# Kernel tuning notes

Hardware: AMD Instinct MI355X
Metric: run time of the kernel (lower is better)

The kernel has to match this reference:

```python
import jax, jax.numpy as jnp
import numpy as np

EPS = 1e-5
INV_SQRT2 = 0.7071067811865476

def _rmsnorm(x, w):
    rms = jnp.sqrt(jnp.sum(x * x, axis=-1) / x.shape[-1] + EPS)
    return x / rms[..., None] * w

def _gelu(x):
    # exact erf-based GELU as in the torch module
    return x * (1.0 + jax.scipy.special.erf(x * INV_SQRT2)) * 0.5

def setup_inputs() -> dict:
    key = jax.random.key(0)
    ks = jax.random.split(key, 8)
    B, S, D, DFF = 4, 2048, 1024, 4096
    s = 0.02  # realistic init scale keeps softmax non-degenerate
    return {
        "x": jax.random.normal(ks[0], (B, S, D), jnp.float32),
        "ln1": jax.random.uniform(ks[1], (D,), jnp.float32),
        "ln2": jax.random.uniform(ks[2], (D,), jnp.float32),
        "ffn1": jax.random.normal(ks[3], (DFF, D), jnp.float32) * s,
        "ffn2": jax.random.normal(ks[4], (D, DFF), jnp.float32) * s,
        "k_proj": jax.random.normal(ks[5], (D, D), jnp.float32) * s,
        "q_proj": jax.random.normal(ks[6], (D, D), jnp.float32) * s,
        "v_proj": jax.random.normal(ks[7], (D, D), jnp.float32) * s,
        "out_proj": jax.random.normal(jax.random.fold_in(key, 99), (D, D), jnp.float32) * s,
    }

def reference(x, ln1, ln2, ffn1, ffn2, k_proj, q_proj, v_proj, out_proj):
    S = x.shape[1]
    d_k = x.shape[-1]
    # --- attention branch (single-head, as in source) ---
    h = _rmsnorm(x, ln1)
    Q = h @ q_proj.T  # [B,S,D]
    K = h @ k_proj.T
    V = h @ v_proj.T
    scores = jnp.einsum('bqd,bkd->bqk', Q, K) / jnp.sqrt(jnp.float32(d_k))
    attn = jax.nn.softmax(scores, axis=-1)
    # source: softmax first, then zero out strict-upper (future) entries, renormalize
    causal = jnp.tril(jnp.ones((S, S), jnp.float32))
    attn = attn * causal
    attn = attn / jnp.sum(attn, axis=-1, keepdims=True)
    mh = jnp.einsum('bqk,bkd->bqd', attn, V) @ out_proj
    y = x + mh
    # --- FFN branch: NOTE source feeds RMSNorm2(x), not y ---
    h2 = _rmsnorm(x, ln2)
    ff = _gelu(h2 @ ffn1.T) @ ffn2.T
    return y + ff
```

## Files before the change

kernel.cpp:

```cpp
#include <hip/hip_runtime.h>
#include <math.h>

typedef __bf16 bf16_t;
typedef __bf16 bf16x8 __attribute__((ext_vector_type(8)));
typedef float f32x4 __attribute__((ext_vector_type(4)));

#define LDS16(g, l) __builtin_amdgcn_global_load_lds( \
    (__attribute__((address_space(1))) void*)(g),     \
    (__attribute__((address_space(3))) void*)(l), 16, 0, 0)

__global__ __launch_bounds__(256) void prep_kernel(
    const float* __restrict__ qp, const float* __restrict__ kp,
    const float* __restrict__ vp, const float* __restrict__ f1,
    const float* __restrict__ f2, const float* __restrict__ op,
    const float* __restrict__ x, const float* __restrict__ ln1,
    bf16_t* __restrict__ qkvb, bf16_t* __restrict__ f1b,
    bf16_t* __restrict__ f2b, bf16_t* __restrict__ opT,
    bf16_t* __restrict__ h1)
{
    __shared__ float tile[32][33];
    __shared__ float red[4];
    int bid = blockIdx.x;
    int t = threadIdx.x;
    if (bid < 11264) {
        size_t i = ((size_t)bid * 256 + t) * 4;
        const float* src;
        bf16_t* dst;
        if (i < 3145728) {
            if (i < 1048576)      { src = qp + i;             dst = qkvb + i; }
            else if (i < 2097152) { src = kp + (i - 1048576); dst = qkvb + i; }
            else                  { src = vp + (i - 2097152); dst = qkvb + i; }
        } else if (i < 7340032) { src = f1 + (i - 3145728); dst = f1b + (i - 3145728); }
        else                    { src = f2 + (i - 7340032); dst = f2b + (i - 7340032); }
        float4 v = *(const float4*)src;
        dst[0] = (bf16_t)v.x; dst[1] = (bf16_t)v.y;
        dst[2] = (bf16_t)v.z; dst[3] = (bf16_t)v.w;
    } else if (bid < 12288) {
        int b2 = bid - 11264;
        int c0 = (b2 & 31) * 32, r0 = (b2 >> 5) * 32;
        int tx = t & 31, ty = t >> 5;
#pragma unroll
        for (int i = 0; i < 32; i += 8)
            tile[ty + i][tx] = op[(size_t)(r0 + ty + i) * 1024 + c0 + tx];
        __syncthreads();
#pragma unroll
        for (int i = 0; i < 32; i += 8)
            opT[(size_t)(c0 + ty + i) * 1024 + r0 + tx] = (bf16_t)tile[tx][ty + i];
    } else {
        int row = bid - 12288;
        float4 xv = ((const float4*)(x + (size_t)row * 1024))[t];
        float ss = xv.x * xv.x + xv.y * xv.y + xv.z * xv.z + xv.w * xv.w;
#pragma unroll
        for (int o = 32; o > 0; o >>= 1) ss += __shfl_xor(ss, o, 64);
        if ((t & 63) == 0) red[t >> 6] = ss;
        __syncthreads();
        ss = red[0] + red[1] + red[2] + red[3];
        float rinv = rsqrtf(ss * (1.0f / 1024.0f) + 1e-5f);
        float4 wv = ((const float4*)ln1)[t];
        bf16_t* hp = h1 + (size_t)row * 1024 + t * 4;
        hp[0] = (bf16_t)(xv.x * rinv * wv.x);
        hp[1] = (bf16_t)(xv.y * rinv * wv.y);
        hp[2] = (bf16_t)(xv.z * rinv * wv.z);
        hp[3] = (bf16_t)(xv.w * rinv * wv.w);
    }
}

__global__ __launch_bounds__(256) void rmsnorm_kernel(
    const float* __restrict__ x, const float* __restrict__ w,
    bf16_t* __restrict__ h)
{
    int row = blockIdx.x;
    int t = threadIdx.x;
    float4 xv = ((const float4*)(x + (size_t)row * 1024))[t];
    float ss = xv.x * xv.x + xv.y * xv.y + xv.z * xv.z + xv.w * xv.w;
#pragma unroll
    for (int o = 32; o > 0; o >>= 1) ss += __shfl_xor(ss, o, 64);
    __shared__ float red[4];
    if ((t & 63) == 0) red[t >> 6] = ss;
    __syncthreads();
    ss = red[0] + red[1] + red[2] + red[3];
    float rinv = rsqrtf(ss * (1.0f / 1024.0f) + 1e-5f);
    float4 wv = ((const float4*)w)[t];
    bf16_t* hp = h + (size_t)row * 1024 + t * 4;
    hp[0] = (bf16_t)(xv.x * rinv * wv.x);
    hp[1] = (bf16_t)(xv.y * rinv * wv.y);
    hp[2] = (bf16_t)(xv.z * rinv * wv.z);
    hp[3] = (bf16_t)(xv.w * rinv * wv.w);
}

__global__ __launch_bounds__(256) void transpose_bf16(
    const bf16_t* __restrict__ in, bf16_t* __restrict__ out,
    int rows, int ldin, long long sIn, long long sOut)
{
    __shared__ bf16_t tile[32][33];
    int b = blockIdx.z;
    const bf16_t* ip = in + (long long)b * sIn;
    bf16_t* op = out + (long long)b * sOut;
    int c0 = blockIdx.x * 32, r0 = blockIdx.y * 32;
    int tx = threadIdx.x & 31, ty = threadIdx.x >> 5;
#pragma unroll
    for (int i = 0; i < 32; i += 8)
        tile[ty + i][tx] = ip[(size_t)(r0 + ty + i) * ldin + c0 + tx];
    __syncthreads();
#pragma unroll
    for (int i = 0; i < 32; i += 8)
        op[(size_t)(c0 + ty + i) * rows + r0 + tx] = tile[tx][ty + i];
}

__global__ __launch_bounds__(256) void causal_softmax_kernel(bf16_t* __restrict__ SP)
{
    const int S = 2048;
    int q = blockIdx.x, b = blockIdx.y;
    bf16_t* row = SP + ((size_t)b * S + q) * S;
    int t = threadIdx.x;
    int j0 = t * 8;
    int Jstore = ((q >> 7) + 1) << 7;

    float v[8];
    if (j0 + 7 <= q) {
        bf16x8 xv = *(const bf16x8*)(row + j0);
#pragma unroll
        for (int i = 0; i < 8; i++) v[i] = (float)xv[i];
    } else if (j0 <= q) {
#pragma unroll
        for (int i = 0; i < 8; i++)
            v[i] = (j0 + i <= q) ? (float)row[j0 + i] : -1e30f;
    } else {
#pragma unroll
        for (int i = 0; i < 8; i++) v[i] = -1e30f;
    }

    float mx = v[0];
#pragma unroll
    for (int i = 1; i < 8; i++) mx = fmaxf(mx, v[i]);
#pragma unroll
    for (int o = 32; o > 0; o >>= 1) mx = fmaxf(mx, __shfl_xor(mx, o, 64));
    __shared__ float sm[4], ssum[4];
    if ((t & 63) == 0) sm[t >> 6] = mx;
    __syncthreads();
    mx = fmaxf(fmaxf(sm[0], sm[1]), fmaxf(sm[2], sm[3]));

    float e[8];
    float sum = 0.f;
#pragma unroll
    for (int i = 0; i < 8; i++) {
        e[i] = (v[i] > -1e29f) ? expf(v[i] - mx) : 0.f;
        sum += e[i];
    }
#pragma unroll
    for (int o = 32; o > 0; o >>= 1) sum += __shfl_xor(sum, o, 64);
    if ((t & 63) == 0) ssum[t >> 6] = sum;
    __syncthreads();
    sum = ssum[0] + ssum[1] + ssum[2] + ssum[3];
    float r = 1.0f / sum;

    if (j0 < Jstore) {
        bf16x8 ov;
#pragma unroll
        for (int i = 0; i < 8; i++) ov[i] = (bf16_t)(e[i] * r);
        *(bf16x8*)(row + j0) = ov;
    }
}

template <int EPI, bool CSKIP, bool CKLOOP, bool ASPLIT>
__global__ __launch_bounds__(256) void gemm_bt(
    const bf16_t* __restrict__ A, const bf16_t* __restrict__ A2, int lda,
    const bf16_t* __restrict__ B, int ldb,
    void* Cv, int ldc, const float* R,
    int K, int Ksp, int Mt, long long sA, long long sB, long long sC,
    float scale)
{
    int id = blockIdx.x, bz = blockIdx.z;
    int xcd = id & 7, p = id >> 3;
    int chunk = Mt >> 3;
    int bm = xcd * chunk + (p % chunk);
    int bn = p / chunk;
    if (CSKIP && bn > bm) return;

    __shared__ __align__(16) bf16_t At[128 * 64];
    __shared__ __align__(16) bf16_t Bt[128 * 64];
    int t = threadIdx.x;
    int w = t >> 6, l = t & 63;
    int wm = w >> 1, wn = w & 1;
    int lane_m = l & 15, quad = l >> 4;

    const bf16_t* Ag = A + (long long)bz * sA + (size_t)(bm * 128) * lda;
    const bf16_t* Bg = B + (long long)bz * sB + (size_t)(bn * 128) * ldb;

    int Keff = K;
    if (CKLOOP) {
        int kk = (bm + 1) * 128;
        if (kk < K) Keff = kk;
    }

    f32x4 acc[4][4] = {};

    int rb = w * 8 + (l >> 3);
    int g0 = ((l & 7) ^ ((l >> 3) & 7)) * 8;
    const bf16_t* a0[4];
    const bf16_t* a1[4];
    const bf16_t* b0[4];
#pragma unroll
    for (int j = 0; j < 4; j++) {
        size_t ro = (size_t)(rb + 32 * j);
        a0[j] = Ag + ro * lda + g0;
        if (ASPLIT) a1[j] = A2 + (long long)bz * sA + (size_t)(bm * 128) * lda
                           + ro * lda + g0;
        b0[j] = Bg + ro * ldb + g0;
    }

    int s0 = (quad ^ (lane_m & 7)) * 8;
    int s1 = ((4 + quad) ^ (lane_m & 7)) * 8;

    for (int kt = 0; kt < Keff; kt += 64) {
        __syncthreads();
#pragma unroll
        for (int j = 0; j < 4; j++) {
            const bf16_t* pa = a0[j] + kt;
            if (ASPLIT && kt >= Ksp) pa = a1[j] + (kt - Ksp);
            LDS16(pa, At + (size_t)w * 512 + j * 2048);
            LDS16(b0[j] + kt, Bt + (size_t)w * 512 + j * 2048);
        }
        __syncthreads();

#pragma unroll
        for (int h = 0; h < 2; h++) {
            int sh = h ? s1 : s0;
            bf16x8 af[4], bfr[4];
#pragma unroll
            for (int mi = 0; mi < 4; mi++)
                af[mi] = *(const bf16x8*)(At + (wm * 64 + mi * 16 + lane_m) * 64 + sh);
#pragma unroll
            for (int ni = 0; ni < 4; ni++)
                bfr[ni] = *(const bf16x8*)(Bt + (wn * 64 + ni * 16 + lane_m) * 64 + sh);
#pragma unroll
            for (int mi = 0; mi < 4; mi++)
#pragma unroll
                for (int ni = 0; ni < 4; ni++)
                    acc[mi][ni] = __builtin_amdgcn_mfma_f32_16x16x32_bf16(
                        af[mi], bfr[ni], acc[mi][ni], 0, 0, 0);
        }
    }

    long long cbase = (long long)bz * sC;
#pragma unroll
    for (int mi = 0; mi < 4; mi++) {
#pragma unroll
        for (int r = 0; r < 4; r++) {
            int row = bm * 128 + wm * 64 + mi * 16 + quad * 4 + r;
#pragma unroll
            for (int ni = 0; ni < 4; ni++) {
                int col = bn * 128 + wn * 64 + ni * 16 + lane_m;
                float v = acc[mi][ni][r];
                size_t idx = (size_t)(cbase + (long long)row * ldc + col);
                if (EPI == 0) {
                    ((bf16_t*)Cv)[idx] = (bf16_t)(v * scale);
                } else if (EPI == 1) {
                    float g = 0.5f * v * (1.0f + erff(v * 0.70710678118654752f));
                    ((bf16_t*)Cv)[idx] = (bf16_t)g;
                } else {
                    float rv = R[(size_t)row * ldc + col];
                    ((float*)Cv)[idx] = v + rv;
                }
            }
        }
    }
}

extern "C" void kernel_launch(void* const* d_in, const int* in_sizes, int n_in,
                              void* d_out, int out_size, void* d_ws, size_t ws_size,
                              hipStream_t stream)
{
    (void)in_sizes; (void)n_in; (void)out_size;
    const float* x    = (const float*)d_in[0];
    const float* ln1  = (const float*)d_in[1];
    const float* ln2  = (const float*)d_in[2];
    const float* ffn1 = (const float*)d_in[3];
    const float* ffn2 = (const float*)d_in[4];
    const float* kp   = (const float*)d_in[5];
    const float* qp   = (const float*)d_in[6];
    const float* vp   = (const float*)d_in[7];
    const float* op   = (const float*)d_in[8];
    float* out = (float*)d_out;

    const size_t MiB = 1048576;
    char* ws = (char*)d_ws;
    bf16_t* qkvb = (bf16_t*)(ws + 0 * MiB);
    bf16_t* opT  = (bf16_t*)(ws + 6 * MiB);
    bf16_t* f1b  = (bf16_t*)(ws + 8 * MiB);
    bf16_t* f2b  = (bf16_t*)(ws + 16 * MiB);
    bf16_t* h1   = (bf16_t*)(ws + 24 * MiB);
    bf16_t* VT   = (bf16_t*)(ws + 24 * MiB);
    bf16_t* h2   = (bf16_t*)(ws + 24 * MiB);
    bf16_t* QKVb = (bf16_t*)(ws + 40 * MiB);
    bf16_t* AV   = (bf16_t*)(ws + 40 * MiB);
    bf16_t* G0   = (bf16_t*)(ws + 40 * MiB);
    bf16_t* G1   = (bf16_t*)(ws + 72 * MiB);
    bf16_t* SP   = (bf16_t*)d_out;
    bool bigws = ws_size >= 104 * MiB;

    dim3 blk(256);
    const int HUGE_K = 1 << 30;

    prep_kernel<<<dim3(20480), blk, 0, stream>>>(
        qp, kp, vp, ffn1, ffn2, op, x, ln1, qkvb, f1b, f2b, opT, h1);

    gemm_bt<0, false, false, false><<<dim3(1536), blk, 0, stream>>>(
        h1, h1, 1024, qkvb, 1024, QKVb, 3072, nullptr,
        1024, HUGE_K, 64, 0, 0, 0, 1.0f);

    gemm_bt<0, true, false, false><<<dim3(256, 1, 4), blk, 0, stream>>>(
        QKVb, QKVb, 3072, QKVb + 1024, 3072, SP, 2048, nullptr,
        1024, HUGE_K, 16,
        (long long)2048 * 3072, (long long)2048 * 3072, (long long)2048 * 2048,
        1.0f / 32.0f);

    transpose_bf16<<<dim3(32, 64, 4), blk, 0, stream>>>(
        QKVb + 2048, VT, 2048, 3072,
        (long long)2048 * 3072, (long long)1024 * 2048);

    causal_softmax_kernel<<<dim3(2048, 4), blk, 0, stream>>>(SP);

    gemm_bt<0, false, true, false><<<dim3(128, 1, 4), blk, 0, stream>>>(
        SP, SP, 2048, VT, 2048, AV, 1024, nullptr,
        2048, HUGE_K, 16,
        (long long)2048 * 2048, (long long)1024 * 2048, (long long)2048 * 1024,
        1.0f);

    gemm_bt<2, false, false, false><<<dim3(512), blk, 0, stream>>>(
        AV, AV, 1024, opT, 1024, out, 1024, x,
        1024, HUGE_K, 64, 0, 0, 0, 1.0f);

    rmsnorm_kernel<<<dim3(8192), blk, 0, stream>>>(x, ln2, h2);

    if (bigws) {
        gemm_bt<1, false, false, false><<<dim3(1024), blk, 0, stream>>>(
            h2, h2, 1024, f1b, 1024, G0, 2048, nullptr,
            1024, HUGE_K, 64, 0, 0, 0, 1.0f);
        gemm_bt<1, false, false, false><<<dim3(1024), blk, 0, stream>>>(
            h2, h2, 1024, f1b + (size_t)2048 * 1024, 1024, G1, 2048, nullptr,
            1024, HUGE_K, 64, 0, 0, 0, 1.0f);
        gemm_bt<2, false, false, true><<<dim3(512), blk, 0, stream>>>(
            G0, G1, 2048, f2b, 4096, out, 1024, out,
            4096, 2048, 64, 0, 0, 0, 1.0f);
    } else {
        for (int half = 0; half < 2; half++) {
            gemm_bt<1, false, false, false><<<dim3(1024), blk, 0, stream>>>(
                h2, h2, 1024, f1b + (size_t)half * 2048 * 1024, 1024, G0, 2048,
                nullptr, 1024, HUGE_K, 64, 0, 0, 0, 1.0f);
            gemm_bt<2, false, false, false><<<dim3(512), blk, 0, stream>>>(
                G0, G0, 2048, f2b + half * 2048, 4096, out, 1024, out,
                2048, HUGE_K, 64, 0, 0, 0, 1.0f);
        }
    }
}
```

Measured before the change: 546.7 us.

## Add 8-wave 256x128 GEMM kernel with XCD-aware mapping for dense projections

Adds a new 512-thread GEMM kernel using 256x128 tiles, double-buffered direct-to-LDS loads interleaved with four MFMA phases, priority raising and an XCD-aware block-to-tile mapping. It replaces the QKV, out-projection and FFN GEMMs in the big-workspace path, and merges the two FFN1 halves into a single launch writing a contiguous G buffer. Larger tiles raise operand reuse and the interleaved prefetch aims to hide global latency. The cost is more LDS and registers per block and reliance on hardcoded grid shapes matching M/N.

```diff
diff --git a/kernel.cpp b/kernel.cpp
--- a/kernel.cpp
+++ b/kernel.cpp
@@ -267,6 +267,165 @@
     }
 }
 
+template <int EPI>
+__global__ __launch_bounds__(512, 2) void gemm8p(
+    const bf16_t* __restrict__ A, int lda,
+    const bf16_t* __restrict__ B, int ldb,
+    void* Cv, int ldc, const float* R, int K, float scale)
+{
+    int id = blockIdx.x;
+    int xcd = id & 7, p = id >> 3;
+    int bm = xcd * 4 + (p & 3);
+    int bn = p >> 2;
+
+    __shared__ __align__(16) bf16_t As[2][256 * 64];
+    __shared__ __align__(16) bf16_t Bs[2][128 * 64];
+
+    int t = threadIdx.x;
+    int w = t >> 6, l = t & 63;
+    int wm = w >> 1, wn = w & 1;
+    int lane_m = l & 15, quad = l >> 4;
+
+    const bf16_t* Ag = A + (size_t)(bm * 256) * lda;
+    const bf16_t* Bg = B + (size_t)(bn * 128) * ldb;
+
+    int rsub = w * 8 + (l >> 3);
+    int g0 = ((l & 7) ^ ((l >> 3) & 7)) * 8;
+    const bf16_t* pA0 = Ag + (size_t)(rsub)       * lda + g0;
+    const bf16_t* pA1 = Ag + (size_t)(64 + rsub)  * lda + g0;
+    const bf16_t* pA2 = Ag + (size_t)(128 + rsub) * lda + g0;
+    const bf16_t* pA3 = Ag + (size_t)(192 + rsub) * lda + g0;
+    const bf16_t* pB0 = Bg + (size_t)(rsub)       * ldb + g0;
+    const bf16_t* pB1 = Bg + (size_t)(64 + rsub)  * ldb + g0;
+
+    int sl0 = (quad ^ (lane_m & 7)) * 8;
+    int sl1 = ((4 + quad) ^ (lane_m & 7)) * 8;
+    int arow = (wm * 64 + lane_m) * 64;
+    int brow = (wn * 64 + lane_m) * 64;
+
+    f32x4 acc[4][4] = {};
+
+    LDS16(pA0, &As[0][0 * 4096 + w * 512]);
+    LDS16(pA1, &As[0][1 * 4096 + w * 512]);
+    LDS16(pA2, &As[0][2 * 4096 + w * 512]);
+    LDS16(pA3, &As[0][3 * 4096 + w * 512]);
+    LDS16(pB0, &Bs[0][0 * 4096 + w * 512]);
+    LDS16(pB1, &Bs[0][1 * 4096 + w * 512]);
+    asm volatile("s_waitcnt vmcnt(0)" ::: "memory");
+    __builtin_amdgcn_s_barrier();
+
+    int cur = 0;
+    for (int kt = 0; kt < K; kt += 64) {
+        const bool pf = (kt + 64) < K;
+        const int nxt = cur ^ 1;
+        const bf16_t* Ac = As[cur];
+        const bf16_t* Bc = Bs[cur];
+        bf16x8 af[2], bfr0[4], bfr1[4];
+
+        af[0] = *(const bf16x8*)(Ac + arow + 0 * 1024 + sl0);
+        af[1] = *(const bf16x8*)(Ac + arow + 1 * 1024 + sl0);
+#pragma unroll
+        for (int ni = 0; ni < 4; ni++)
+            bfr0[ni] = *(const bf16x8*)(Bc + brow + ni * 1024 + sl0);
+        if (pf) {
+            LDS16(pA0 + kt + 64, &As[nxt][0 * 4096 + w * 512]);
+            LDS16(pA1 + kt + 64, &As[nxt][1 * 4096 + w * 512]);
+            LDS16(pA2 + kt + 64, &As[nxt][2 * 4096 + w * 512]);
+            LDS16(pA3 + kt + 64, &As[nxt][3 * 4096 + w * 512]);
+        }
+        __builtin_amdgcn_s_barrier();
+        asm volatile("s_waitcnt lgkmcnt(0)" ::: "memory");
+        __builtin_amdgcn_sched_barrier(0);
+        __builtin_amdgcn_s_setprio(1);
+#pragma unroll
+        for (int j = 0; j < 2; j++)
+#pragma unroll
+            for (int ni = 0; ni < 4; ni++)
+                acc[j][ni] = __builtin_amdgcn_mfma_f32_16x16x32_bf16(
+                    af[j], bfr0[ni], acc[j][ni], 0, 0, 0);
+        __builtin_amdgcn_s_setprio(0);
+        __builtin_amdgcn_s_barrier();
+
+        af[0] = *(const bf16x8*)(Ac + arow + 0 * 1024 + sl1);
+        af[1] = *(const bf16x8*)(Ac + arow + 1 * 1024 + sl1);
+#pragma unroll
+        for (int ni = 0; ni < 4; ni++)
+            bfr1[ni] = *(const bf16x8*)(Bc + brow + ni * 1024 + sl1);
+        if (pf) {
+            LDS16(pB0 + kt + 64, &Bs[nxt][0 * 4096 + w * 512]);
+            LDS16(pB1 + kt + 64, &Bs[nxt][1 * 4096 + w * 512]);
+        }
+        __builtin_amdgcn_s_barrier();
+        asm volatile("s_waitcnt lgkmcnt(0)" ::: "memory");
+        __builtin_amdgcn_sched_barrier(0);
+        __builtin_amdgcn_s_setprio(1);
+#pragma unroll
+        for (int j = 0; j < 2; j++)
+#pragma unroll
+            for (int ni = 0; ni < 4; ni++)
+                acc[j][ni] = __builtin_amdgcn_mfma_f32_16x16x32_bf16(
+                    af[j], bfr1[ni], acc[j][ni], 0, 0, 0);
+        __builtin_amdgcn_s_setprio(0);
+        __builtin_amdgcn_s_barrier();
+
+        af[0] = *(const bf16x8*)(Ac + arow + 2 * 1024 + sl0);
+        af[1] = *(const bf16x8*)(Ac + arow + 3 * 1024 + sl0);
+        __builtin_amdgcn_s_barrier();
+        asm volatile("s_waitcnt lgkmcnt(0)" ::: "memory");
+        __builtin_amdgcn_sched_barrier(0);
+        __builtin_amdgcn_s_setprio(1);
+#pragma unroll
+        for (int j = 0; j < 2; j++)
+#pragma unroll
+            for (int ni = 0; ni < 4; ni++)
+                acc[2 + j][ni] = __builtin_amdgcn_mfma_f32_16x16x32_bf16(
+                    af[j], bfr0[ni], acc[2 + j][ni], 0, 0, 0);
+        __builtin_amdgcn_s_setprio(0);
+        __builtin_amdgcn_s_barrier();
+
+        af[0] = *(const bf16x8*)(Ac + arow + 2 * 1024 + sl1);
+        af[1] = *(const bf16x8*)(Ac + arow + 3 * 1024 + sl1);
+        __builtin_amdgcn_s_barrier();
+        asm volatile("s_waitcnt lgkmcnt(0)" ::: "memory");
+        __builtin_amdgcn_sched_barrier(0);
+        __builtin_amdgcn_s_setprio(1);
+#pragma unroll
+        for (int j = 0; j < 2; j++)
+#pragma unroll
+            for (int ni = 0; ni < 4; ni++)
+                acc[2 + j][ni] = __builtin_amdgcn_mfma_f32_16x16x32_bf16(
+                    af[j], bfr1[ni], acc[2 + j][ni], 0, 0, 0);
+        __builtin_amdgcn_s_setprio(0);
+        if (pf) asm volatile("s_waitcnt vmcnt(0)" ::: "memory");
+        __builtin_amdgcn_s_barrier();
+
+        cur = nxt;
+    }
+
+#pragma unroll
+    for (int mi = 0; mi < 4; mi++) {
+#pragma unroll
+        for (int r = 0; r < 4; r++) {
+            int row = bm * 256 + wm * 64 + mi * 16 + quad * 4 + r;
+#pragma unroll
+            for (int ni = 0; ni < 4; ni++) {
+                int col = bn * 128 + wn * 64 + ni * 16 + lane_m;
+                float v = acc[mi][ni][r];
+                size_t idx = (size_t)row * ldc + col;
+                if (EPI == 0) {
+                    ((bf16_t*)Cv)[idx] = (bf16_t)(v * scale);
+                } else if (EPI == 1) {
+                    float g = 0.5f * v * (1.0f + erff(v * 0.70710678118654752f));
+                    ((bf16_t*)Cv)[idx] = (bf16_t)g;
+                } else {
+                    float rv = R[(size_t)row * ldc + col];
+                    ((float*)Cv)[idx] = v + rv;
+                }
+            }
+        }
+    }
+}
+
 extern "C" void kernel_launch(void* const* d_in, const int* in_sizes, int n_in,
                               void* d_out, int out_size, void* d_ws, size_t ws_size,
                               hipStream_t stream)
@@ -295,19 +454,18 @@
     bf16_t* QKVb = (bf16_t*)(ws + 40 * MiB);
     bf16_t* AV   = (bf16_t*)(ws + 40 * MiB);
     bf16_t* G0   = (bf16_t*)(ws + 40 * MiB);
-    bf16_t* G1   = (bf16_t*)(ws + 72 * MiB);
     bf16_t* SP   = (bf16_t*)d_out;
     bool bigws = ws_size >= 104 * MiB;
 
     dim3 blk(256);
+    dim3 blk8(512);
     const int HUGE_K = 1 << 30;
 
     prep_kernel<<<dim3(20480), blk, 0, stream>>>(
         qp, kp, vp, ffn1, ffn2, op, x, ln1, qkvb, f1b, f2b, opT, h1);
 
-    gemm_bt<0, false, false, false><<<dim3(1536), blk, 0, stream>>>(
-        h1, h1, 1024, qkvb, 1024, QKVb, 3072, nullptr,
-        1024, HUGE_K, 64, 0, 0, 0, 1.0f);
+    gemm8p<0><<<dim3(768), blk8, 0, stream>>>(
+        h1, 1024, qkvb, 1024, QKVb, 3072, nullptr, 1024, 1.0f);
 
     gemm_bt<0, true, false, false><<<dim3(256, 1, 4), blk, 0, stream>>>(
         QKVb, QKVb, 3072, QKVb + 1024, 3072, SP, 2048, nullptr,
@@ -327,22 +485,16 @@
         (long long)2048 * 2048, (long long)1024 * 2048, (long long)2048 * 1024,
         1.0f);
 
-    gemm_bt<2, false, false, false><<<dim3(512), blk, 0, stream>>>(
-        AV, AV, 1024, opT, 1024, out, 1024, x,
-        1024, HUGE_K, 64, 0, 0, 0, 1.0f);
+    gemm8p<2><<<dim3(256), blk8, 0, stream>>>(
+        AV, 1024, opT, 1024, out, 1024, x, 1024, 1.0f);
 
     rmsnorm_kernel<<<dim3(8192), blk, 0, stream>>>(x, ln2, h2);
 
     if (bigws) {
-        gemm_bt<1, false, false, false><<<dim3(1024), blk, 0, stream>>>(
-            h2, h2, 1024, f1b, 1024, G0, 2048, nullptr,
-            1024, HUGE_K, 64, 0, 0, 0, 1.0f);
-        gemm_bt<1, false, false, false><<<dim3(1024), blk, 0, stream>>>(
-            h2, h2, 1024, f1b + (size_t)2048 * 1024, 1024, G1, 2048, nullptr,
-            1024, HUGE_K, 64, 0, 0, 0, 1.0f);
-        gemm_bt<2, false, false, true><<<dim3(512), blk, 0, stream>>>(
-            G0, G1, 2048, f2b, 4096, out, 1024, out,
-            4096, 2048, 64, 0, 0, 0, 1.0f);
+        gemm8p<1><<<dim3(1024), blk8, 0, stream>>>(
+            h2, 1024, f1b, 1024, G0, 4096, nullptr, 1024, 1.0f);
+        gemm8p<2><<<dim3(256), blk8, 0, stream>>>(
+            G0, 4096, f2b, 4096, out, 1024, out, 4096, 1.0f);
     } else {
         for (int half = 0; half < 2; half++) {
             gemm_bt<1, false, false, false><<<dim3(1024), blk, 0, stream>>>(
```

Measured after the change: 542.9 us. Within noise of the previous version (-0.7%).

## Add 256x256 tile GEMM with deep async LDS pipeline for projection and FFN GEMMs

Applied to the files above, without the earlier changes.

Introduces a new 512-thread GEMM kernel with 256x256 output tiles, double-buffered split-K LDS staging via global_load_lds, swizzled LDS layout, explicit vmcnt waits, setprio around MFMA blocks, and XCD-aware block remapping. It replaces the old 128-tile gemm_bt for the QKV projection, out-projection and FFN GEMMs, and merges the two FFN1 halves into one launch writing a 4096-wide G0. The aim is better data reuse and overlap of loads with MFMA. The cost is far fewer blocks (128 for the out-projection and FFN2), which may underfill the GPU's CUs. The hand-scheduled waits also risk ordering bugs.

```diff
diff --git a/kernel.cpp b/kernel.cpp
--- a/kernel.cpp
+++ b/kernel.cpp
@@ -267,6 +267,133 @@
     }
 }
 
+#define VM8 asm volatile("s_waitcnt vmcnt(8)" ::: "memory")
+#define VM4 asm volatile("s_waitcnt vmcnt(4)" ::: "memory")
+#define VM0 asm volatile("s_waitcnt vmcnt(0)" ::: "memory")
+#define NOP ((void)0)
+
+#define STAGE_A(BUF, KH, KOFF) do { \
+    LDS16(rA0 + (KOFF), &As[BUF][KH][w * 512]);        \
+    LDS16(rA1 + (KOFF), &As[BUF][KH][4096 + w * 512]); } while (0)
+#define STAGE_B(BUF, KH, KOFF) do { \
+    LDS16(rB0 + (KOFF), &Bs[BUF][KH][w * 512]);        \
+    LDS16(rB1 + (KOFF), &Bs[BUF][KH][4096 + w * 512]); } while (0)
+
+#define PHASE(BUF, KH, MQ, STAGE_STMT, WAIT_STMT)                             \
+  {                                                                           \
+    _Pragma("unroll") for (int mi = 0; mi < 4; mi++)                          \
+        af[mi] = *(const bf16x8*)&As[BUF][KH][arow + (MQ)*2048 + mi*512];     \
+    if ((MQ) == 0) {                                                          \
+      _Pragma("unroll") for (int ni = 0; ni < 4; ni++)                        \
+          bfr[ni] = *(const bf16x8*)&Bs[BUF][KH][brow + ni*512];              \
+    }                                                                         \
+    STAGE_STMT;                                                               \
+    __builtin_amdgcn_s_barrier();                                             \
+    asm volatile("s_waitcnt lgkmcnt(0)" ::: "memory");                        \
+    __builtin_amdgcn_sched_barrier(0);                                        \
+    __builtin_amdgcn_s_setprio(1);                                            \
+    _Pragma("unroll") for (int mi = 0; mi < 4; mi++)                          \
+      _Pragma("unroll") for (int ni = 0; ni < 4; ni++)                        \
+        acc[(MQ)*4 + mi][ni] = __builtin_amdgcn_mfma_f32_16x16x32_bf16(       \
+            af[mi], bfr[ni], acc[(MQ)*4 + mi][ni], 0, 0, 0);                  \
+    __builtin_amdgcn_s_setprio(0);                                            \
+    WAIT_STMT;                                                                \
+    __builtin_amdgcn_s_barrier();                                             \
+  }
+
+template <int EPI>
+__global__ __launch_bounds__(512, 2) void gemm256(
+    const bf16_t* __restrict__ A, int lda,
+    const bf16_t* __restrict__ B, int ldb,
+    void* Cv, int ldc, const float* R, int K, int Nt, float scale)
+{
+    int id = blockIdx.x;
+    int xcd = id & 7, p = id >> 3;
+    int chunk = gridDim.x >> 3;
+    int g = xcd * chunk + p;
+    int bm = g / Nt, bn = g % Nt;
+
+    __shared__ __align__(16) bf16_t As[2][2][256 * 32];
+    __shared__ __align__(16) bf16_t Bs[2][2][256 * 32];
+
+    int t = threadIdx.x;
+    int w = t >> 6, l = t & 63;
+    int wm = w >> 2, wn = w & 3;
+    int lm = l & 15, quad = l >> 4;
+
+    const bf16_t* Ag = A + (size_t)(bm * 256) * lda;
+    const bf16_t* Bg = B + (size_t)(bn * 256) * ldb;
+
+    int g4 = ((l & 3) ^ ((l >> 2) & 3)) * 8;
+    const bf16_t* rA0 = Ag + (size_t)(w * 16 + (l >> 2)) * lda + g4;
+    const bf16_t* rA1 = rA0 + (size_t)128 * lda;
+    const bf16_t* rB0 = Bg + (size_t)(w * 16 + (l >> 2)) * ldb + g4;
+    const bf16_t* rB1 = rB0 + (size_t)128 * ldb;
+
+    int slot8 = (quad ^ (lm & 3)) * 8;
+    int arow = (wm * 128 + lm) * 32 + slot8;
+    int brow = (wn * 64 + lm) * 32 + slot8;
+
+    f32x4 acc[8][4] = {};
+    bf16x8 af[4], bfr[4];
+
+    STAGE_A(0, 0, 0);  STAGE_B(0, 0, 0);
+    STAGE_A(0, 1, 32); STAGE_B(0, 1, 32);
+    STAGE_A(1, 0, 64); STAGE_B(1, 0, 64);
+    VM8;
+    __builtin_amdgcn_s_barrier();
+
+    int T = K >> 7;
+    for (int it = 0; it < T - 1; ++it) {
+        int kb = it << 7;
+        PHASE(0, 0, 0, STAGE_A(1, 1, kb + 96),  NOP);
+        PHASE(0, 0, 1, STAGE_B(1, 1, kb + 96),  VM8);
+        PHASE(0, 1, 0, STAGE_A(0, 0, kb + 128), NOP);
+        PHASE(0, 1, 1, STAGE_B(0, 0, kb + 128), VM8);
+        PHASE(1, 0, 0, STAGE_A(0, 1, kb + 160), NOP);
+        PHASE(1, 0, 1, STAGE_B(0, 1, kb + 160), VM8);
+        PHASE(1, 1, 0, STAGE_A(1, 0, kb + 192), NOP);
+        PHASE(1, 1, 1, STAGE_B(1, 0, kb + 192), VM8);
+    }
+    {
+        int kb = (T - 1) << 7;
+        PHASE(0, 0, 0, STAGE_A(1, 1, kb + 96), NOP);
+        PHASE(0, 0, 1, STAGE_B(1, 1, kb + 96), VM8);
+        PHASE(0, 1, 0, NOP, NOP);
+        PHASE(0, 1, 1, NOP, VM4);
+        PHASE(1, 0, 0, NOP, NOP);
+        PHASE(1, 0, 1, NOP, VM0);
+        PHASE(1, 1, 0, NOP, NOP);
+        PHASE(1, 1, 1, NOP, NOP);
+    }
+
+#pragma unroll
+    for (int mq = 0; mq < 2; mq++) {
+#pragma unroll
+        for (int mi = 0; mi < 4; mi++) {
+#pragma unroll
+            for (int r = 0; r < 4; r++) {
+                int row = bm * 256 + wm * 128 + mq * 64 + mi * 16 + quad * 4 + r;
+#pragma unroll
+                for (int ni = 0; ni < 4; ni++) {
+                    int col = bn * 256 + wn * 64 + ni * 16 + lm;
+                    float v = acc[mq * 4 + mi][ni][r];
+                    size_t idx = (size_t)row * ldc + col;
+                    if (EPI == 0) {
+                        ((bf16_t*)Cv)[idx] = (bf16_t)(v * scale);
+                    } else if (EPI == 1) {
+                        float ge = 0.5f * v * (1.0f + erff(v * 0.70710678118654752f));
+                        ((bf16_t*)Cv)[idx] = (bf16_t)ge;
+                    } else {
+                        float rv = R[(size_t)row * ldc + col];
+                        ((float*)Cv)[idx] = v + rv;
+                    }
+                }
+            }
+        }
+    }
+}
+
 extern "C" void kernel_launch(void* const* d_in, const int* in_sizes, int n_in,
                               void* d_out, int out_size, void* d_ws, size_t ws_size,
                               hipStream_t stream)
@@ -295,19 +422,18 @@
     bf16_t* QKVb = (bf16_t*)(ws + 40 * MiB);
     bf16_t* AV   = (bf16_t*)(ws + 40 * MiB);
     bf16_t* G0   = (bf16_t*)(ws + 40 * MiB);
-    bf16_t* G1   = (bf16_t*)(ws + 72 * MiB);
     bf16_t* SP   = (bf16_t*)d_out;
     bool bigws = ws_size >= 104 * MiB;
 
     dim3 blk(256);
+    dim3 blk5(512);
     const int HUGE_K = 1 << 30;
 
     prep_kernel<<<dim3(20480), blk, 0, stream>>>(
         qp, kp, vp, ffn1, ffn2, op, x, ln1, qkvb, f1b, f2b, opT, h1);
 
-    gemm_bt<0, false, false, false><<<dim3(1536), blk, 0, stream>>>(
-        h1, h1, 1024, qkvb, 1024, QKVb, 3072, nullptr,
-        1024, HUGE_K, 64, 0, 0, 0, 1.0f);
+    gemm256<0><<<dim3(384), blk5, 0, stream>>>(
+        h1, 1024, qkvb, 1024, QKVb, 3072, nullptr, 1024, 12, 1.0f);
 
     gemm_bt<0, true, false, false><<<dim3(256, 1, 4), blk, 0, stream>>>(
         QKVb, QKVb, 3072, QKVb + 1024, 3072, SP, 2048, nullptr,
@@ -327,22 +453,16 @@
         (long long)2048 * 2048, (long long)1024 * 2048, (long long)2048 * 1024,
         1.0f);
 
-    gemm_bt<2, false, false, false><<<dim3(512), blk, 0, stream>>>(
-        AV, AV, 1024, opT, 1024, out, 1024, x,
-        1024, HUGE_K, 64, 0, 0, 0, 1.0f);
+    gemm256<2><<<dim3(128), blk5, 0, stream>>>(
+        AV, 1024, opT, 1024, out, 1024, x, 1024, 4, 1.0f);
 
     rmsnorm_kernel<<<dim3(8192), blk, 0, stream>>>(x, ln2, h2);
 
     if (bigws) {
-        gemm_bt<1, false, false, false><<<dim3(1024), blk, 0, stream>>>(
-            h2, h2, 1024, f1b, 1024, G0, 2048, nullptr,
-            1024, HUGE_K, 64, 0, 0, 0, 1.0f);
-        gemm_bt<1, false, false, false><<<dim3(1024), blk, 0, stream>>>(
-            h2, h2, 1024, f1b + (size_t)2048 * 1024, 1024, G1, 2048, nullptr,
-            1024, HUGE_K, 64, 0, 0, 0, 1.0f);
-        gemm_bt<2, false, false, true><<<dim3(512), blk, 0, stream>>>(
-            G0, G1, 2048, f2b, 4096, out, 1024, out,
-            4096, 2048, 64, 0, 0, 0, 1.0f);
+        gemm256<1><<<dim3(512), blk5, 0, stream>>>(
+            h2, 1024, f1b, 1024, G0, 4096, nullptr, 1024, 16, 1.0f);
+        gemm256<2><<<dim3(128), blk5, 0, stream>>>(
+            G0, 4096, f2b, 4096, out, 1024, out, 4096, 4, 1.0f);
     } else {
         for (int half = 0; half < 2; half++) {
             gemm_bt<1, false, false, false><<<dim3(1024), blk, 0, stream>>>(
```

Result: slower. 595.2 us (+8.9%).
